# Kernel optimization log

Hardware: AMD Instinct MI355X
Metric: run time of the kernel (lower is better)

Reference implementation:

```python
import jax, jax.numpy as jnp
import numpy as np

H_IMG, W_IMG = 64, 64          # token grid (n = H*W = 4096)
D_MODEL = 512
N_HEADS = 8
D1 = 1024                      # expand_ratio * d_model, multiple of n_heads
HEAD_DIM = D1 // N_HEADS       # 128
RANK = 32
NK = 16                        # inducing points for SKI interpolation


def interp_weights(n, nk):
    # inverse-time warp: position i -> 1/(i+1) in (0,1], linearly interpolated
    # onto nk uniform inducing points in [0,1] (2 nonzeros per row).
    pos = 1.0 / (jnp.arange(n, dtype=jnp.float32) + 1.0)
    t = pos * (nk - 1)
    idx = jnp.clip(jnp.floor(t).astype(jnp.int32), 0, nk - 2)
    frac = t - idx.astype(jnp.float32)
    r = jnp.arange(n)
    Wm = jnp.zeros((n, nk), jnp.float32)
    Wm = Wm.at[r, idx].set(1.0 - frac).at[r, idx + 1].set(frac)
    return Wm  # (n, nk)


def apply_toep(v, U, V):
    # v: (b, m, n, h, d); low-rank SKI Toeplitz mixing along axis n.
    # T ~= (Wm @ U) (Wm @ V)^T per head  -> O(n*r*d) instead of O(n^2*d).
    n = v.shape[2]
    nk = U.shape[1]
    Wm = interp_weights(n, nk)                      # (n, nk)
    A = jnp.einsum('nk,hkr->hnr', Wm, U)            # (h, n, r)
    B = jnp.einsum('nk,hkr->hnr', Wm, V)            # (h, n, r)
    tmp = jnp.einsum('hnr,bmnhd->bmhrd', B, v)      # contract over n
    return jnp.einsum('hnr,bmhrd->bmnhd', A, tmp)


def setup_inputs() -> dict:
    key = jax.random.key(0)
    ks = jax.random.split(key, 12)
    s = 0.02
    x = jax.random.normal(ks[0], (16, H_IMG * W_IMG, D_MODEL), jnp.float32)
    Wu = s * jax.random.normal(ks[1], (D1, D_MODEL), jnp.float32)
    bu = s * jax.random.normal(ks[2], (D1,), jnp.float32)
    Wv = s * jax.random.normal(ks[3], (D1, D_MODEL), jnp.float32)
    bv = s * jax.random.normal(ks[4], (D1,), jnp.float32)
    Wo = s * jax.random.normal(ks[5], (D_MODEL, D1), jnp.float32)
    bo = s * jax.random.normal(ks[6], (D_MODEL,), jnp.float32)
    U1 = s * jax.random.normal(ks[7], (N_HEADS, NK, RANK), jnp.float32)
    V1 = s * jax.random.normal(ks[8], (N_HEADS, NK, RANK), jnp.float32)
    U2 = s * jax.random.normal(ks[9], (N_HEADS, NK, RANK), jnp.float32)
    V2 = s * jax.random.normal(ks[10], (N_HEADS, NK, RANK), jnp.float32)
    return {'x': x, 'Wu': Wu, 'bu': bu, 'Wv': Wv, 'bv': bv, 'Wo': Wo,
            'bo': bo, 'U1': U1, 'V1': V1, 'U2': U2, 'V2': V2}


def reference(x, Wu, bu, Wv, bv, Wo, bo, U1, V1, U2, V2):
    b, n, _ = x.shape
    H = int(np.sqrt(n)); W = n // H
    u = jax.nn.silu(x @ Wu.T + bu)                  # (b, n, d1)
    v = jax.nn.silu(x @ Wv.T + bv)                  # (b, n, d1)
    v4 = v.reshape(b, H, W, N_HEADS, HEAD_DIM)      # (b, H, W, h, d)

    # o1: toep1 along W, then toep2 along H
    t = apply_toep(v4, U1, V1)                      # mix along W
    t = t.transpose(0, 2, 1, 3, 4)                  # (b, W, H, h, d)
    t = apply_toep(t, U2, V2)                       # mix along H
    o1 = t.transpose(0, 2, 1, 3, 4)

    # o2: toep2 along H, then toep1 along W
    s_ = v4.transpose(0, 2, 1, 3, 4)                # (b, W, H, h, d)
    s_ = apply_toep(s_, U2, V2)                     # mix along H
    s_ = s_.transpose(0, 2, 1, 3, 4)                # (b, H, W, h, d)
    o2 = apply_toep(s_, U1, V1)                     # mix along W

    out = (o1 + o2).reshape(b, n, D1)
    out = u * out                                   # gated token mixing
    return out @ Wo.T + bo                          # (b, n, d_model)
```

## Files before the change

kernel.cpp:

```cpp
#include <hip/hip_runtime.h>
#include <hip/hip_bf16.h>

typedef unsigned short u16;
typedef unsigned int   u32;
typedef float  f32x4  __attribute__((ext_vector_type(4)));
typedef __bf16 bf16x8 __attribute__((ext_vector_type(8)));
typedef u16    u16x8  __attribute__((ext_vector_type(8)));
typedef u16    u16x4  __attribute__((ext_vector_type(4)));

__device__ __forceinline__ u16 f2bf(float f) {
  u32 x = __builtin_bit_cast(u32, f);
  x += 0x7fffu + ((x >> 16) & 1u);
  return (u16)(x >> 16);
}
__device__ __forceinline__ float bf2f(u16 u) {
  return __builtin_bit_cast(float, (u32)u << 16);
}
__device__ __forceinline__ void gload_lds16(const u16* g, u16* l) {
  __builtin_amdgcn_global_load_lds(
      (const __attribute__((address_space(1))) void*)g,
      (__attribute__((address_space(3))) void*)l, 16, 0, 0);
}

__global__ void k_conv_x(const float* __restrict__ x, u16* __restrict__ xb) {
  int g = blockIdx.x * 256 + threadIdx.x;
  const float4* src = (const float4*)(x + (size_t)g * 8);
  float4 f0 = src[0], f1 = src[1];
  u16x8 o;
  o[0]=f2bf(f0.x); o[1]=f2bf(f0.y); o[2]=f2bf(f0.z); o[3]=f2bf(f0.w);
  o[4]=f2bf(f1.x); o[5]=f2bf(f1.y); o[6]=f2bf(f1.z); o[7]=f2bf(f1.w);
  *(u16x8*)(xb + (size_t)g * 8) = o;
}

__global__ void k_conv_w(const float* __restrict__ Wu, const float* __restrict__ Wv,
                         const float* __restrict__ Wo, const float* __restrict__ bu,
                         const float* __restrict__ bv, u16* __restrict__ wuvb,
                         u16* __restrict__ wob, float* __restrict__ biasuv) {
  int g = blockIdx.x * 256 + threadIdx.x;
  int e = g * 4;
  const float* src; u16* dst;
  if (e < 524288)        { src = Wu + e;             dst = wuvb + e; }
  else if (e < 1048576)  { src = Wv + (e - 524288);  dst = wuvb + e; }
  else                   { src = Wo + (e - 1048576); dst = wob + (e - 1048576); }
  float4 f = *(const float4*)src;
  u16x4 o; o[0]=f2bf(f.x); o[1]=f2bf(f.y); o[2]=f2bf(f.z); o[3]=f2bf(f.w);
  *(u16x4*)dst = o;
  if (g < 2048) biasuv[g] = (g < 1024) ? bu[g] : bv[g - 1024];
}

__global__ void k_toep(const float* __restrict__ U1, const float* __restrict__ V1,
                       const float* __restrict__ U2, const float* __restrict__ V2,
                       u16* __restrict__ T1b, u16* __restrict__ T2b) {
  __shared__ float Us[512], Vs[512];
  int bid = blockIdx.x, t = threadIdx.x;
  int which = bid >> 6, rest = bid & 63, h = rest >> 3, seg = rest & 7;
  const float* U = which ? U2 : U1;
  const float* V = which ? V2 : V1;
  u16* T = which ? T2b : T1b;
  float scale = which ? 2.0f : 1.0f;
  for (int i = t; i < 512; i += 256) { Us[i] = U[h*512 + i]; Vs[i] = V[h*512 + i]; }
  __syncthreads();
  for (int q = 0; q < 2; ++q) {
    int e = seg * 512 + q * 256 + t;
    int i = e >> 6, j = e & 63;
    float pi = 1.0f / (float)(i + 1); float tvi = pi * 15.0f;
    int ii = min((int)floorf(tvi), 14); float fi = tvi - (float)ii;
    float pj = 1.0f / (float)(j + 1); float tvj = pj * 15.0f;
    int jj = min((int)floorf(tvj), 14); float fj = tvj - (float)jj;
    float s = 0.0f;
    #pragma unroll
    for (int r = 0; r < 32; ++r) {
      float a = (1.0f - fi) * Us[ii*32 + r] + fi * Us[(ii+1)*32 + r];
      float b = (1.0f - fj) * Vs[jj*32 + r] + fj * Vs[(jj+1)*32 + r];
      s += a * b;
    }
    T[h*4096 + i*64 + j] = f2bf(s * scale);
  }
}

template<int EPI>
__global__ __launch_bounds__(256) void k_gemm(const u16* __restrict__ A,
    const u16* __restrict__ B, const float* __restrict__ bias,
    void* __restrict__ C, int K, int nbn, int ldc) {
  __shared__ alignas(16) u16 As[128 * 64];
  __shared__ alignas(16) u16 Bs[128 * 64];
  int bid = blockIdx.x;
  int bm = bid / nbn, bn = bid % nbn;
  int t = threadIdx.x, l = t & 63, w = t >> 6;
  const u16* Ab = A + (size_t)bm * 128 * K;
  const u16* Bb = B + (size_t)bn * 128 * K;
  f32x4 acc[4][4];
  #pragma unroll
  for (int i = 0; i < 4; ++i)
    #pragma unroll
    for (int j = 0; j < 4; ++j) acc[i][j] = (f32x4){0.f, 0.f, 0.f, 0.f};
  int wm = (w >> 1) * 64, wn = (w & 1) * 64;
  for (int kt = 0; kt < K; kt += 64) {
    #pragma unroll
    for (int q = 0; q < 4; ++q) {
      int c = q * 256 + t;
      int row = c >> 3, col = (c & 7) * 8;
      gload_lds16(Ab + (size_t)row * K + kt + col, &As[c * 8]);
    }
    #pragma unroll
    for (int q = 0; q < 4; ++q) {
      int c = q * 256 + t;
      int row = c >> 3, col = (c & 7) * 8;
      gload_lds16(Bb + (size_t)row * K + kt + col, &Bs[c * 8]);
    }
    __syncthreads();
    #pragma unroll
    for (int ks = 0; ks < 2; ++ks) {
      bf16x8 af[4], bfr[4];
      #pragma unroll
      for (int mf = 0; mf < 4; ++mf)
        af[mf] = *(const bf16x8*)&As[(wm + mf*16 + (l & 15)) * 64 + ks*32 + (l >> 4)*8];
      #pragma unroll
      for (int nf = 0; nf < 4; ++nf)
        bfr[nf] = *(const bf16x8*)&Bs[(wn + nf*16 + (l & 15)) * 64 + ks*32 + (l >> 4)*8];
      #pragma unroll
      for (int mf = 0; mf < 4; ++mf)
        #pragma unroll
        for (int nf = 0; nf < 4; ++nf)
          acc[mf][nf] = __builtin_amdgcn_mfma_f32_16x16x32_bf16(af[mf], bfr[nf], acc[mf][nf], 0, 0, 0);
    }
    __syncthreads();
  }
  #pragma unroll
  for (int mf = 0; mf < 4; ++mf) {
    int gm0 = bm * 128 + wm + mf * 16 + (l >> 4) * 4;
    #pragma unroll
    for (int nf = 0; nf < 4; ++nf) {
      int gn = bn * 128 + wn + nf * 16 + (l & 15);
      float bi = bias[gn];
      #pragma unroll
      for (int r = 0; r < 4; ++r) {
        float z = acc[mf][nf][r] + bi;
        size_t off = (size_t)(gm0 + r) * ldc + gn;
        if (EPI == 0) {
          z = z / (1.0f + __expf(-z));
          ((u16*)C)[off] = f2bf(z);
        } else {
          ((float*)C)[off] = z;
        }
      }
    }
  }
}

template<int PASS>
__global__ __launch_bounds__(256) void k_mix(const u16* __restrict__ uv,
                                             u16* __restrict__ y,
                                             const u16* __restrict__ Tmat) {
  __shared__ alignas(16) u16 Ts[64 * 72];
  __shared__ alignas(16) u32 VT[128 * 36];
  int bid = blockIdx.x, t = threadIdx.x;
  int h = bid & 7, outer = (bid >> 3) & 63, b = bid >> 9;
  int l = t & 63, w = t >> 6;

  {
    const u16* Tg = Tmat + h * 4096;
    int rr = t >> 2, cc = (t & 3) * 16;
    const uint4* src = (const uint4*)(Tg + rr * 64 + cc);
    uint4 v0 = src[0], v1 = src[1];
    *(uint4*)&Ts[rr * 72 + cc] = v0;
    *(uint4*)&Ts[rr * 72 + cc + 8] = v1;
  }

  size_t inbase; size_t instride;
  if (PASS == 0) { inbase = ((size_t)(b*64 + outer) * 64) * 2048 + 1024 + h*128; instride = 2048; }
  else           { inbase = ((size_t)b * 4096 + outer) * 1024 + h*128;            instride = 65536; }
  const u16* inp = (PASS == 0) ? uv : (const u16*)y;

  #pragma unroll
  for (int a2 = 0; a2 < 2; ++a2) {
    int jp = (t >> 4) + a2 * 16;
    int dc = t & 15;
    const u16* r0 = inp + inbase + (size_t)(2*jp) * instride + dc * 8;
    const u16* r1 = r0 + instride;
    uint4 av = *(const uint4*)r0;
    uint4 bv = *(const uint4*)r1;
    u32 a4[4] = {av.x, av.y, av.z, av.w};
    u32 b4[4] = {bv.x, bv.y, bv.z, bv.w};
    #pragma unroll
    for (int ww = 0; ww < 4; ++ww) {
      u32 lo = (a4[ww] & 0xffffu) | (b4[ww] << 16);
      u32 hi = (a4[ww] >> 16) | (b4[ww] & 0xffff0000u);
      int d0 = dc * 8 + 2 * ww, d1 = d0 + 1;
      VT[d0 * 36 + (jp ^ ((((u32)d0 >> 3) & 7) << 2))] = lo;
      VT[d1 * 36 + (jp ^ ((((u32)d1 >> 3) & 7) << 2))] = hi;
    }
  }
  __syncthreads();

  f32x4 acc[8];
  #pragma unroll
  for (int nf = 0; nf < 8; ++nf) acc[nf] = (f32x4){0.f, 0.f, 0.f, 0.f};
  #pragma unroll
  for (int ks = 0; ks < 2; ++ks) {
    bf16x8 af = *(const bf16x8*)&Ts[(w*16 + (l & 15)) * 72 + ks*32 + (l >> 4)*8];
    #pragma unroll
    for (int nf = 0; nf < 8; ++nf) {
      int d  = nf * 16 + (l & 15);
      int kd = ks * 16 + (l >> 4) * 4;
      u32 dw = (u32)d * 36 + ((u32)kd ^ ((((u32)d >> 3) & 7) << 2));
      bf16x8 bfv = *(const bf16x8*)&VT[dw];
      acc[nf] = __builtin_amdgcn_mfma_f32_16x16x32_bf16(af, bfv, acc[nf], 0, 0, 0);
    }
  }

  size_t obase, ostride, ubase = 0;
  if (PASS == 0) { obase = ((size_t)(b*64 + outer) * 64) * 1024 + h*128; ostride = 1024; }
  else {
    obase = ((size_t)b * 4096 + outer) * 1024 + h*128; ostride = 65536;
    ubase = ((size_t)b * 4096 + outer) * 2048 + h*128;
  }
  #pragma unroll
  for (int nf = 0; nf < 8; ++nf) {
    int d = nf * 16 + (l & 15);
    #pragma unroll
    for (int r = 0; r < 4; ++r) {
      int m = w * 16 + (l >> 4) * 4 + r;
      float val = acc[nf][r];
      if (PASS == 1) val *= bf2f(uv[ubase + (size_t)m * 131072 + d]);
      y[obase + (size_t)m * ostride + d] = f2bf(val);
    }
  }
}

extern "C" void kernel_launch(void* const* d_in, const int* in_sizes, int n_in,
                              void* d_out, int out_size, void* d_ws, size_t ws_size,
                              hipStream_t stream) {
  const float* x  = (const float*)d_in[0];
  const float* Wu = (const float*)d_in[1];
  const float* bu = (const float*)d_in[2];
  const float* Wv = (const float*)d_in[3];
  const float* bv = (const float*)d_in[4];
  const float* Wo = (const float*)d_in[5];
  const float* bo = (const float*)d_in[6];
  const float* U1 = (const float*)d_in[7];
  const float* V1 = (const float*)d_in[8];
  const float* U2 = (const float*)d_in[9];
  const float* V2 = (const float*)d_in[10];
  float* out = (float*)d_out;

  char* p = (char*)d_ws;
  u16*  xb     = (u16*)(p + 0);
  u16*  wuvb   = (u16*)(p + 67108864);
  u16*  wob    = (u16*)(p + 69206016);
  u16*  T1b    = (u16*)(p + 70254592);
  u16*  T2b    = (u16*)(p + 70320128);
  float* biasuv= (float*)(p + 70385664);
  u16*  uv     = (u16*)(p + 70393856);
  u16*  y      = (u16*)(p + 338829312);
  if (ws_size < 473047040ULL) return;

  k_conv_x<<<16384, 256, 0, stream>>>(x, xb);
  k_conv_w<<<1536, 256, 0, stream>>>(Wu, Wv, Wo, bu, bv, wuvb, wob, biasuv);
  k_toep<<<128, 256, 0, stream>>>(U1, V1, U2, V2, T1b, T2b);
  k_gemm<0><<<8192, 256, 0, stream>>>(xb, wuvb, biasuv, (void*)uv, 512, 16, 2048);
  k_mix<0><<<8192, 256, 0, stream>>>(uv, y, T1b);
  k_mix<1><<<8192, 256, 0, stream>>>(uv, y, T2b);
  k_gemm<1><<<2048, 256, 0, stream>>>(y, wob, bo, (void*)out, 1024, 4, 512);
}
```

Measured before the change: 619.3 us.

## Replace GEMM with 256x256 tiled, double-buffered, swizzled-LDS pipelined kernel

Replaces the 128x128 single-buffered bf16 MFMA GEMM with a 256x256 tile kernel using 512 threads and 128KB of dynamic LDS split into two buffers. Global-to-LDS loads for the next K tile are issued in quarter-tile stages interleaved with MFMA compute, using vmcnt waits and s_setprio to overlap memory with math. LDS rows are XOR-swizzled to avoid bank conflicts, and block indices are remapped across groups of eight for better L2 locality. The larger tile raises data reuse, but it also means fewer workgroups and higher register and LDS pressure, and the waitcnt/barrier schedule must be exactly right.

```diff
diff --git a/kernel.cpp b/kernel.cpp
--- a/kernel.cpp
+++ b/kernel.cpp
@@ -79,63 +79,113 @@
 }
 
 template<int EPI>
-__global__ __launch_bounds__(256) void k_gemm(const u16* __restrict__ A,
-    const u16* __restrict__ B, const float* __restrict__ bias,
-    void* __restrict__ C, int K, int nbn, int ldc) {
-  __shared__ alignas(16) u16 As[128 * 64];
-  __shared__ alignas(16) u16 Bs[128 * 64];
-  int bid = blockIdx.x;
-  int bm = bid / nbn, bn = bid % nbn;
-  int t = threadIdx.x, l = t & 63, w = t >> 6;
-  const u16* Ab = A + (size_t)bm * 128 * K;
-  const u16* Bb = B + (size_t)bn * 128 * K;
-  f32x4 acc[4][4];
-  #pragma unroll
-  for (int i = 0; i < 4; ++i)
+__global__ __launch_bounds__(512, 2) void k_gemm256(
+    const u16* __restrict__ A, const u16* __restrict__ B,
+    const float* __restrict__ bias, void* __restrict__ C,
+    int K, int nbn, int ldc) {
+  extern __shared__ uint4 smem4[];
+  u16* lds = (u16*)smem4;
+  const int t = threadIdx.x;
+  const int l = t & 63, w = t >> 6;
+  const int wmi = w >> 2, wni = w & 3;
+  const int nwg = gridDim.x;
+  const int lb = (blockIdx.x & 7) * (nwg >> 3) + (blockIdx.x >> 3);
+  const int bm = lb / nbn, bn = lb % nbn;
+  const u16* Ab = A + (size_t)bm * 256 * K;
+  const u16* Bb = B + (size_t)bn * 256 * K;
+  const int NT = K >> 6;
+  const int NOPS = NT * 4;
+
+  f32x4 acc[8][4];
+  #pragma unroll
+  for (int i = 0; i < 8; ++i)
     #pragma unroll
     for (int j = 0; j < 4; ++j) acc[i][j] = (f32x4){0.f, 0.f, 0.f, 0.f};
-  int wm = (w >> 1) * 64, wn = (w & 1) * 64;
-  for (int kt = 0; kt < K; kt += 64) {
-    #pragma unroll
-    for (int q = 0; q < 4; ++q) {
-      int c = q * 256 + t;
-      int row = c >> 3, col = (c & 7) * 8;
-      gload_lds16(Ab + (size_t)row * K + kt + col, &As[c * 8]);
-    }
-    #pragma unroll
-    for (int q = 0; q < 4; ++q) {
-      int c = q * 256 + t;
-      int row = c >> 3, col = (c & 7) * 8;
-      gload_lds16(Bb + (size_t)row * K + kt + col, &Bs[c * 8]);
-    }
-    __syncthreads();
-    #pragma unroll
-    for (int ks = 0; ks < 2; ++ks) {
-      bf16x8 af[4], bfr[4];
+
+#define STAGE(gop) do {                                                      \
+    int _g = (gop);                                                          \
+    int _tile = _g >> 2, _half = _g & 3;                                     \
+    int _kt = _tile << 6;                                                    \
+    const u16* _src = (_half < 2) ? Ab : Bb;                                 \
+    int _rowbase = (_half & 1) << 7;                                         \
+    u16* _dst = lds + (_tile & 1) * 32768 + ((_half >= 2) ? 16384 : 0)       \
+                + _rowbase * 64;                                             \
+    _Pragma("unroll")                                                        \
+    for (int _j = 0; _j < 2; ++_j) {                                         \
+      int _idx = _j * 512 + t;                                               \
+      int _rr = _idx >> 3, _s8 = _idx & 7;                                   \
+      int _R = _rowbase + _rr;                                               \
+      int _col = (_s8 ^ (_R & 7)) << 3;                                      \
+      gload_lds16(_src + (size_t)_R * K + _kt + _col, _dst + _idx * 8);      \
+    }                                                                        \
+  } while (0)
+
+  #pragma unroll
+  for (int g = 0; g < 7; ++g) STAGE(g);
+  asm volatile("s_waitcnt vmcnt(6)");
+  __builtin_amdgcn_s_barrier();
+
+  for (int tile = 0; tile < NT; ++tile) {
+    const int buf = tile & 1;
+    const u16* As = lds + buf * 32768;
+    const u16* Bs = As + 16384;
+    #pragma unroll
+    for (int p = 0; p < 4; ++p) {
+      const int mq = (p >> 1) * 4, nq = (p & 1) * 2;
+      bf16x8 af[8], bfv[4];
       #pragma unroll
-      for (int mf = 0; mf < 4; ++mf)
-        af[mf] = *(const bf16x8*)&As[(wm + mf*16 + (l & 15)) * 64 + ks*32 + (l >> 4)*8];
+      for (int ks = 0; ks < 2; ++ks) {
+        #pragma unroll
+        for (int i = 0; i < 4; ++i) {
+          int R = (wmi << 7) + (mq + i) * 16 + (l & 15);
+          int q8 = ks * 4 + (l >> 4);
+          af[ks*4+i] = *(const bf16x8*)&As[R * 64 + ((q8 ^ (R & 7)) << 3)];
+        }
+        #pragma unroll
+        for (int i = 0; i < 2; ++i) {
+          int R = (wni << 6) + (nq + i) * 16 + (l & 15);
+          int q8 = ks * 4 + (l >> 4);
+          bfv[ks*2+i] = *(const bf16x8*)&Bs[R * 64 + ((q8 ^ (R & 7)) << 3)];
+        }
+      }
+      {
+        int g = 7 + tile * 4 + p;
+        if (g < NOPS) STAGE(g);
+      }
+      if (p == 3) {
+        if (tile < NT - 2)        asm volatile("s_waitcnt vmcnt(6)");
+        else if (tile == NT - 2)  asm volatile("s_waitcnt vmcnt(0)");
+      }
+      __builtin_amdgcn_s_barrier();
+      asm volatile("s_waitcnt lgkmcnt(0)");
+      __builtin_amdgcn_s_setprio(1);
       #pragma unroll
-      for (int nf = 0; nf < 4; ++nf)
-        bfr[nf] = *(const bf16x8*)&Bs[(wn + nf*16 + (l & 15)) * 64 + ks*32 + (l >> 4)*8];
-      #pragma unroll
-      for (int mf = 0; mf < 4; ++mf)
+      for (int ks = 0; ks < 2; ++ks)
         #pragma unroll
-        for (int nf = 0; nf < 4; ++nf)
-          acc[mf][nf] = __builtin_amdgcn_mfma_f32_16x16x32_bf16(af[mf], bfr[nf], acc[mf][nf], 0, 0, 0);
-    }
-    __syncthreads();
-  }
-  #pragma unroll
-  for (int mf = 0; mf < 4; ++mf) {
-    int gm0 = bm * 128 + wm + mf * 16 + (l >> 4) * 4;
+        for (int i = 0; i < 4; ++i)
+          #pragma unroll
+          for (int j = 0; j < 2; ++j)
+            acc[mq+i][nq+j] = __builtin_amdgcn_mfma_f32_16x16x32_bf16(
+                af[ks*4+i], bfv[ks*2+j], acc[mq+i][nq+j], 0, 0, 0);
+      __builtin_amdgcn_s_setprio(0);
+      __builtin_amdgcn_s_barrier();
+    }
+  }
+#undef STAGE
+
+  float bcol[4];
+  #pragma unroll
+  for (int nf = 0; nf < 4; ++nf)
+    bcol[nf] = bias[bn * 256 + (wni << 6) + nf * 16 + (l & 15)];
+  #pragma unroll
+  for (int mf = 0; mf < 8; ++mf) {
+    int gm0 = bm * 256 + (wmi << 7) + mf * 16 + (l >> 4) * 4;
     #pragma unroll
     for (int nf = 0; nf < 4; ++nf) {
-      int gn = bn * 128 + wn + nf * 16 + (l & 15);
-      float bi = bias[gn];
+      int gn = bn * 256 + (wni << 6) + nf * 16 + (l & 15);
       #pragma unroll
       for (int r = 0; r < 4; ++r) {
-        float z = acc[mf][nf][r] + bi;
+        float z = acc[mf][nf][r] + bcol[nf];
         size_t off = (size_t)(gm0 + r) * ldc + gn;
         if (EPI == 0) {
           z = z / (1.0f + __expf(-z));
@@ -255,11 +305,16 @@
   u16*  y      = (u16*)(p + 338829312);
   if (ws_size < 473047040ULL) return;
 
+  (void)hipFuncSetAttribute((const void*)&k_gemm256<0>,
+      hipFuncAttributeMaxDynamicSharedMemorySize, 131072);
+  (void)hipFuncSetAttribute((const void*)&k_gemm256<1>,
+      hipFuncAttributeMaxDynamicSharedMemorySize, 131072);
+
   k_conv_x<<<16384, 256, 0, stream>>>(x, xb);
   k_conv_w<<<1536, 256, 0, stream>>>(Wu, Wv, Wo, bu, bv, wuvb, wob, biasuv);
   k_toep<<<128, 256, 0, stream>>>(U1, V1, U2, V2, T1b, T2b);
-  k_gemm<0><<<8192, 256, 0, stream>>>(xb, wuvb, biasuv, (void*)uv, 512, 16, 2048);
+  k_gemm256<0><<<2048, 512, 131072, stream>>>(xb, wuvb, biasuv, (void*)uv, 512, 8, 2048);
   k_mix<0><<<8192, 256, 0, stream>>>(uv, y, T1b);
   k_mix<1><<<8192, 256, 0, stream>>>(uv, y, T2b);
-  k_gemm<1><<<2048, 256, 0, stream>>>(y, wob, bo, (void*)out, 1024, 4, 512);
-}
+  k_gemm256<1><<<512, 512, 131072, stream>>>(y, wob, bo, (void*)out, 1024, 2, 512);
+}
```

After: 546.9 us. 1.13x faster.
